# Kernel tuning notes

Measured on AMD Instinct MI355X. Metric: run time of the kernel, lower is better.

Reference implementation:

```python
import jax, jax.numpy as jnp
import numpy as np

EPS = 1e-8


def box2corners(box):
    # box: (B, N, 5) = (x, y, w, h, alpha) -> corners (B, N, 4, 2)
    x, y, w, h, alpha = (box[..., i] for i in range(5))
    x4 = jnp.asarray([0.5, -0.5, -0.5, 0.5], box.dtype) * w[..., None]   # (B,N,4)
    y4 = jnp.asarray([0.5, 0.5, -0.5, -0.5], box.dtype) * h[..., None]
    c = jnp.cos(alpha)[..., None]
    s = jnp.sin(alpha)[..., None]
    cx = x4 * c - y4 * s + x[..., None]
    cy = x4 * s + y4 * c + y[..., None]
    return jnp.stack([cx, cy], axis=-1)


def _cross2(a, b):
    return a[..., 0] * b[..., 1] - a[..., 1] * b[..., 0]


def box_intersection(corners1, corners2):
    # pairwise segment intersections of the 4 edges of each box: (B,N,16,2), mask (B,N,16)
    q1 = jnp.roll(corners1, -1, axis=2)
    q2 = jnp.roll(corners2, -1, axis=2)
    p1 = corners1[:, :, :, None, :]          # (B,N,4,1,2)
    r = (q1 - corners1)[:, :, :, None, :]    # edge dirs of box1
    p2 = corners2[:, :, None, :, :]          # (B,N,1,4,2)
    s = (q2 - corners2)[:, :, None, :, :]    # edge dirs of box2
    den = _cross2(r, s)                      # (B,N,4,4)
    dp = p2 - p1
    t = _cross2(dp, s) / (den + EPS)
    u = _cross2(dp, r) / (den + EPS)
    mask = (t > 0.0) & (t < 1.0) & (u > 0.0) & (u < 1.0)
    inter = (p1 + t[..., None] * r) * mask[..., None]
    B, N = corners1.shape[:2]
    return inter.reshape(B, N, 16, 2), mask.reshape(B, N, 16)


def box_in_box(pts, box):
    # check whether the 4 corners `pts` (B,N,4,2) lie inside rectangle `box` (B,N,4,2)
    a = box[:, :, 0:1, :]
    ab = box[:, :, 1:2, :] - a
    ad = box[:, :, 3:4, :] - a
    am = pts - a
    pab = (am * ab).sum(-1) / (ab * ab).sum(-1)
    pad = (am * ad).sum(-1) / (ad * ad).sum(-1)
    e = 1e-6
    return (pab > -e) & (pab < 1 + e) & (pad > -e) & (pad < 1 + e)


def oriented_box_intersection_2d(corners1, corners2):
    inter, inter_mask = box_intersection(corners1, corners2)
    c1_in_2 = box_in_box(corners1, corners2)
    c2_in_1 = box_in_box(corners2, corners1)
    vertices = jnp.concatenate([corners1, corners2, inter], axis=2)   # (B,N,24,2)
    mask = jnp.concatenate([c1_in_2, c2_in_1, inter_mask], axis=2)    # (B,N,24) bool
    num_valid = mask.sum(-1)                                           # (B,N) int
    mean = (vertices * mask[..., None]).sum(axis=2, keepdims=True) / \
        jnp.maximum(num_valid[..., None, None], 1).astype(vertices.dtype)
    v = (vertices - mean) * mask[..., None]   # invalid -> zero vectors
    ang = jnp.where(mask, jnp.arctan2(v[..., 1], v[..., 0]), 1e3)  # invalid pushed to end
    order = jnp.argsort(ang, axis=-1)
    vs = jnp.take_along_axis(v, order[..., None], axis=2)  # valid CCW-sorted, zeros after
    # shoelace over consecutive pairs; zero rows contribute nothing
    total = (vs[..., :-1, 0] * vs[..., 1:, 1] - vs[..., 1:, 0] * vs[..., :-1, 1]).sum(-1)
    # close the polygon: cross(v_last_valid, v_first)
    idx_last = jnp.maximum(num_valid - 1, 0)[..., None, None]
    v_last = jnp.take_along_axis(vs, jnp.broadcast_to(idx_last, (*vs.shape[:2], 1, 2)), axis=2)[:, :, 0]
    v0 = vs[:, :, 0]
    total = total + (v_last[..., 0] * v0[..., 1] - v0[..., 0] * v_last[..., 1])
    return jnp.abs(total) * 0.5, vs


def diff_iou_rotated_3d(box3d1, box3d2):
    box1 = box3d1[..., jnp.array([0, 1, 3, 4, 6])]
    box2 = box3d2[..., jnp.array([0, 1, 3, 4, 6])]
    corners1 = box2corners(box1)
    corners2 = box2corners(box2)
    inter_2d, _ = oriented_box_intersection_2d(corners1, corners2)
    zmax1 = box3d1[..., 2] + box3d1[..., 5] * 0.5
    zmin1 = box3d1[..., 2] - box3d1[..., 5] * 0.5
    zmax2 = box3d2[..., 2] + box3d2[..., 5] * 0.5
    zmin2 = box3d2[..., 2] - box3d2[..., 5] * 0.5
    z_overlap = jnp.clip(jnp.minimum(zmax1, zmax2) - jnp.maximum(zmin1, zmin2), 0.0, None)
    inter_3d = inter_2d * z_overlap
    vol1 = box3d1[..., 3] * box3d1[..., 4] * box3d1[..., 5]
    vol2 = box3d2[..., 3] * box3d2[..., 4] * box3d2[..., 5]
    union_3d = vol1 + vol2 - inter_3d
    return inter_3d / union_3d


def setup_inputs() -> dict:
    key = jax.random.key(0)
    k1, k2 = jax.random.split(key)
    N = 1_000_000
    pred = jax.random.uniform(k1, (N, 7), dtype=jnp.float32)
    target = jax.random.uniform(k2, (N, 7), dtype=jnp.float32)
    return {"pred": pred, "target": target}


def reference(pred, target):
    # RotatedIoU3DLoss(mode='iou', reduction='mean', loss_weight=1.0), weight=None
    iou = diff_iou_rotated_3d(pred[None], target[None])[0]  # (N,)
    return 1.0 * jnp.mean(1.0 - iou)
```

## Files before the change

### kernel.cpp

```cpp
#include <hip/hip_runtime.h>
#include <math.h>

__device__ __forceinline__ float frcp(float x) { return __builtin_amdgcn_rcpf(x); }

__device__ __forceinline__ float edge_area(float px, float py, float qx, float qy,
                                           float hw, float hh) {
    const float Y0 = -hh, Y1 = hh;
    float dx = qx - px, dy = qy - py;
    float lo = fmaxf(fminf(px, qx), -hw);
    float hi = fminf(fmaxf(px, qx),  hw);
    float w  = hi - lo;
    float dys = (fabsf(dy) > 1e-20f) ? dy : ((dy >= 0.f) ? 1e-20f : -1e-20f);
    float dxs = (fabsf(dx) > 1e-20f) ? dx : ((dx >= 0.f) ? 1e-20f : -1e-20f);
    float xdy = dx * frcp(dys);
    float m   = dy * frcp(dxs);
    float xa = fmaf(Y0 - py, xdy, px);
    float xb = fmaf(Y1 - py, xdy, px);
    float s0 = fminf(xa, xb), s1 = fmaxf(xa, xb);
    float u0 = fminf(fmaxf(s0, lo), hi);
    float u1 = fminf(fmaxf(s1, lo), hi);
    float yu0 = fmaf(m, u0 - px, py);
    float yu1 = fmaf(m, u1 - px, py);
    yu0 = fminf(fmaxf(yu0, Y0), Y1);
    yu1 = fminf(fmaxf(yu1, Y0), Y1);
    bool mpos = (dy >= 0.f) == (dx >= 0.f);
    float YL = mpos ? Y0 : Y1;
    float YR = mpos ? Y1 : Y0;
    float integral = YL * (u0 - lo)
                   + 0.5f * (yu0 + yu1) * (u1 - u0)
                   + YR * (hi - u1);
    float contrib = integral - Y0 * w;
    float res = (dx > 0.f) ? -contrib : contrib;
    return (w > 0.f) ? res : 0.f;
}

__device__ __forceinline__ float elem_loss(const float b1[7], const float b2[7]) {
    float x1 = b1[0], y1 = b1[1], z1 = b1[2], w1 = b1[3], h1 = b1[4], dz1 = b1[5], a1 = b1[6];
    float x2 = b2[0], y2 = b2[1], z2 = b2[2], w2 = b2[3], h2 = b2[4], dz2 = b2[5], a2 = b2[6];

    float zo = fmaxf(fminf(z1 + 0.5f * dz1, z2 + 0.5f * dz2)
                   - fmaxf(z1 - 0.5f * dz1, z2 - 0.5f * dz2), 0.0f);
    float vol1 = w1 * h1 * dz1;
    float vol2 = w2 * h2 * dz2;

    float sa = __sinf(a2), ca = __cosf(a2);
    float dxc = x1 - x2, dyc = y1 - y2;
    float tx =  dxc * ca + dyc * sa;
    float ty = -dxc * sa + dyc * ca;
    float ad = a1 - a2;
    float sd = __sinf(ad), cd = __cosf(ad);
    float hw1 = 0.5f * w1, hh1 = 0.5f * h1;
    float hw2 = 0.5f * w2, hh2 = 0.5f * h2;
    float ex = hw1 * cd, ey = hw1 * sd;
    float fx = -hh1 * sd, fy = hh1 * cd;
    float q0x = tx + ex + fx, q0y = ty + ey + fy;
    float q1x = tx - ex + fx, q1y = ty - ey + fy;
    float q2x = tx - ex - fx, q2y = ty - ey - fy;
    float q3x = tx + ex - fx, q3y = ty + ey - fy;

    float area = edge_area(q0x, q0y, q1x, q1y, hw2, hh2)
               + edge_area(q1x, q1y, q2x, q2y, hw2, hh2)
               + edge_area(q2x, q2y, q3x, q3y, hw2, hh2)
               + edge_area(q3x, q3y, q0x, q0y, hw2, hh2);
    area = fabsf(area);

    float inter3d = area * zo;
    float union3d = vol1 + vol2 - inter3d;
    return 1.0f - inter3d / union3d;
}

#define WAVES 4

__global__ __launch_bounds__(256) void iou3d_loss_kernel(
    const float* __restrict__ pred, const float* __restrict__ target,
    float* __restrict__ partial, int N)
{
    __shared__ float lds[WAVES][1792];
    const int lane = threadIdx.x & 63;
    const int wid  = threadIdx.x >> 6;
    const long gw  = (long)blockIdx.x * WAVES + wid;
    const long eb  = gw * 128;
    const long totF2 = ((long)N * 7) >> 1;

    const float2* pred2 = (const float2*)pred;
    const float2* targ2 = (const float2*)target;
    float2* ldsP = (float2*)&lds[wid][0];
    float2* ldsT = (float2*)&lds[wid][896];

    float val = 0.f;

    const long f2b = (eb * 7) >> 1;
    #pragma unroll
    for (int k = 0; k < 7; k++) {
        long idx = f2b + k * 64 + lane;
        bool ok = idx < totF2;
        float2 v = ok ? pred2[idx] : make_float2(0.f, 0.f);
        float2 u = ok ? targ2[idx] : make_float2(0.f, 0.f);
        ldsP[k * 64 + lane] = v;
        ldsT[k * 64 + lane] = u;
    }
    float2 va[7], vb[7];
    #pragma unroll
    for (int j = 0; j < 7; j++) {
        va[j] = ldsP[7 * lane + j];
        vb[j] = ldsT[7 * lane + j];
    }
    float af[14], bf[14];
    #pragma unroll
    for (int j = 0; j < 7; j++) {
        af[2 * j] = va[j].x; af[2 * j + 1] = va[j].y;
        bf[2 * j] = vb[j].x; bf[2 * j + 1] = vb[j].y;
    }
    long e0 = eb + 2 * lane;
    if (e0 < N)     val += elem_loss(&af[0], &bf[0]);
    if (e0 + 1 < N) val += elem_loss(&af[7], &bf[7]);

    #pragma unroll
    for (int off = 32; off > 0; off >>= 1)
        val += __shfl_down(val, off, 64);
    __shared__ float wsum[WAVES];
    if (lane == 0) wsum[wid] = val;
    __syncthreads();
    if (threadIdx.x == 0) {
        float s = 0.f;
        #pragma unroll
        for (int q = 0; q < WAVES; q++) s += wsum[q];
        partial[blockIdx.x] = s;
    }
}

__global__ __launch_bounds__(1024) void iou3d_finalize_kernel(
    const float* __restrict__ partial, float* __restrict__ out, int nb, int N)
{
    float s = 0.f;
    for (int i = threadIdx.x; i < nb; i += 1024) s += partial[i];
    #pragma unroll
    for (int off = 32; off > 0; off >>= 1)
        s += __shfl_down(s, off, 64);
    __shared__ float ws[16];
    int lane = threadIdx.x & 63, wid = threadIdx.x >> 6;
    if (lane == 0) ws[wid] = s;
    __syncthreads();
    if (threadIdx.x == 0) {
        float t = 0.f;
        #pragma unroll
        for (int q = 0; q < 16; q++) t += ws[q];
        out[0] = (float)((double)t / (double)N);
    }
}

extern "C" void kernel_launch(void* const* d_in, const int* in_sizes, int n_in,
                              void* d_out, int out_size, void* d_ws, size_t ws_size,
                              hipStream_t stream) {
    const float* pred   = (const float*)d_in[0];
    const float* target = (const float*)d_in[1];
    int N = in_sizes[0] / 7;
    float* partial = (float*)d_ws;

    int grid = (N + 511) / 512;
    iou3d_loss_kernel<<<grid, 256, 0, stream>>>(pred, target, partial, N);
    iou3d_finalize_kernel<<<1, 1024, 0, stream>>>(partial, (float*)d_out, grid, N);
}
```

Baseline: 22.15 us.

## Process multiple tiles per wave with register-prefetched next tile loads

```diff
diff --git a/kernel.cpp b/kernel.cpp
--- a/kernel.cpp
+++ b/kernel.cpp
@@ -66,10 +66,12 @@
 
     float inter3d = area * zo;
     float union3d = vol1 + vol2 - inter3d;
-    return 1.0f - inter3d / union3d;
+    return 1.0f - inter3d * frcp(union3d);
 }
 
 #define WAVES 4
+#define TILES 4
+#define TILE_ELEMS 128
 
 __global__ __launch_bounds__(256) void iou3d_loss_kernel(
     const float* __restrict__ pred, const float* __restrict__ target,
@@ -79,7 +81,7 @@
     const int lane = threadIdx.x & 63;
     const int wid  = threadIdx.x >> 6;
     const long gw  = (long)blockIdx.x * WAVES + wid;
-    const long eb  = gw * 128;
+    const long tile0 = gw * TILES;
     const long totF2 = ((long)N * 7) >> 1;
 
     const float2* pred2 = (const float2*)pred;
@@ -89,31 +91,47 @@
 
     float val = 0.f;
 
-    const long f2b = (eb * 7) >> 1;
-    #pragma unroll
-    for (int k = 0; k < 7; k++) {
-        long idx = f2b + k * 64 + lane;
-        bool ok = idx < totF2;
-        float2 v = ok ? pred2[idx] : make_float2(0.f, 0.f);
-        float2 u = ok ? targ2[idx] : make_float2(0.f, 0.f);
-        ldsP[k * 64 + lane] = v;
-        ldsT[k * 64 + lane] = u;
+    float2 pa[7], pb[7];
+    {
+        const long f2b = tile0 * 448;
+        #pragma unroll
+        for (int k = 0; k < 7; k++) {
+            long idx = f2b + k * 64 + lane;
+            bool ok = idx < totF2;
+            pa[k] = ok ? pred2[idx] : make_float2(0.f, 0.f);
+            pb[k] = ok ? targ2[idx] : make_float2(0.f, 0.f);
+        }
     }
-    float2 va[7], vb[7];
-    #pragma unroll
-    for (int j = 0; j < 7; j++) {
-        va[j] = ldsP[7 * lane + j];
-        vb[j] = ldsT[7 * lane + j];
+
+    #pragma unroll 1
+    for (int t = 0; t < TILES; t++) {
+        #pragma unroll
+        for (int k = 0; k < 7; k++) {
+            ldsP[k * 64 + lane] = pa[k];
+            ldsT[k * 64 + lane] = pb[k];
+        }
+        if (t + 1 < TILES) {
+            const long f2b = (tile0 + t + 1) * 448;
+            #pragma unroll
+            for (int k = 0; k < 7; k++) {
+                long idx = f2b + k * 64 + lane;
+                bool ok = idx < totF2;
+                pa[k] = ok ? pred2[idx] : make_float2(0.f, 0.f);
+                pb[k] = ok ? targ2[idx] : make_float2(0.f, 0.f);
+            }
+        }
+        float af[14], bf[14];
+        #pragma unroll
+        for (int j = 0; j < 7; j++) {
+            float2 va = ldsP[7 * lane + j];
+            float2 vb = ldsT[7 * lane + j];
+            af[2 * j] = va.x; af[2 * j + 1] = va.y;
+            bf[2 * j] = vb.x; bf[2 * j + 1] = vb.y;
+        }
+        long e0 = (tile0 + t) * TILE_ELEMS + 2 * lane;
+        if (e0 < N)     val += elem_loss(&af[0], &bf[0]);
+        if (e0 + 1 < N) val += elem_loss(&af[7], &bf[7]);
     }
-    float af[14], bf[14];
-    #pragma unroll
-    for (int j = 0; j < 7; j++) {
-        af[2 * j] = va[j].x; af[2 * j + 1] = va[j].y;
-        bf[2 * j] = vb[j].x; bf[2 * j + 1] = vb[j].y;
-    }
-    long e0 = eb + 2 * lane;
-    if (e0 < N)     val += elem_loss(&af[0], &bf[0]);
-    if (e0 + 1 < N) val += elem_loss(&af[7], &bf[7]);
 
     #pragma unroll
     for (int off = 32; off > 0; off >>= 1)
@@ -157,7 +175,9 @@
     int N = in_sizes[0] / 7;
     float* partial = (float*)d_ws;
 
-    int grid = (N + 511) / 512;
+    long tiles = ((long)N + TILE_ELEMS - 1) / TILE_ELEMS;
+    long waves = (tiles + TILES - 1) / TILES;
+    int grid = (int)((waves + WAVES - 1) / WAVES);
     iou3d_loss_kernel<<<grid, 256, 0, stream>>>(pred, target, partial, N);
     iou3d_finalize_kernel<<<1, 1024, 0, stream>>>(partial, (float*)d_out, grid, N);
 }
```

Measured after the change: 20.11 us. 1.1x faster.
